# Kernel tuning notes

Measured on AMD Instinct MI355X. Metric: run time of the kernel, lower is better.

## Reference

```python
import jax, jax.numpy as jnp
import numpy as np

EPS = 1e-5

def _layernorm(x, gamma, beta):
    mu = jnp.mean(x, axis=-1, keepdims=True)
    var = jnp.var(x, axis=-1, keepdims=True)
    return (x - mu) * jax.lax.rsqrt(var + EPS) * gamma + beta

def setup_inputs() -> dict:
    key = jax.random.key(0)
    ks = jax.random.split(key, 8)
    B, N, c_z, c_h = 1, 384, 128, 128
    s_z = 1.0 / np.sqrt(c_z)
    s_h = 1.0 / np.sqrt(c_h)
    return {
        "z_ij": jax.random.normal(ks[0], (B, N, N, c_z), dtype=jnp.float32),
        "ln_in_g": jnp.ones((c_z,), jnp.float32),
        "ln_in_b": jnp.zeros((c_z,), jnp.float32),
        "ln_out_g": jnp.ones((c_h,), jnp.float32),
        "ln_out_b": jnp.zeros((c_h,), jnp.float32),
        "Wa1": jax.random.uniform(ks[1], (c_h, c_z), jnp.float32, -s_z, s_z),
        "Wa2": jax.random.uniform(ks[2], (c_h, c_z), jnp.float32, -s_z, s_z),
        "Wb1": jax.random.uniform(ks[3], (c_h, c_z), jnp.float32, -s_z, s_z),
        "Wb2": jax.random.uniform(ks[4], (c_h, c_z), jnp.float32, -s_z, s_z),
        "Wg": jax.random.uniform(ks[5], (c_z, c_z), jnp.float32, -s_z, s_z),
        "Wout": jax.random.uniform(ks[6], (c_z, c_h), jnp.float32, -s_h, s_h),
    }

def reference(z_ij, ln_in_g, ln_in_b, ln_out_g, ln_out_b, Wa1, Wa2, Wb1, Wb2, Wg, Wout):
    # Algorithm 12: triangular multiplicative update, "outgoing" edges
    z = _layernorm(z_ij, ln_in_g, ln_in_b)              # [B,N,N,c_z]
    a = jax.nn.sigmoid(z @ Wa1.T) * (z @ Wa2.T)         # [B,N,N,c_h]
    b = jax.nn.sigmoid(z @ Wb1.T) * (z @ Wb2.T)         # [B,N,N,c_h]
    g = jax.nn.sigmoid(z @ Wg.T)                        # [B,N,N,c_z]
    s = jnp.einsum('bikd,bjkd->bijd', a, b)             # pairwise contraction over k
    return g * (_layernorm(s, ln_out_g, ln_out_b) @ Wout.T)
```

## Files before the change

kernel.cpp:

```cpp
#include <hip/hip_runtime.h>
#include <stdint.h>

#define N 384
#define NR (N*N)
#define PL (NR + 64)
#define C 128
#define WSZ 16384

typedef unsigned short ushort_t;
typedef __attribute__((ext_vector_type(8))) _Float16 f16x8;
typedef __attribute__((ext_vector_type(4))) float f32x4;

__device__ __forceinline__ ushort_t f2h(float f) {
  union { _Float16 h; ushort_t u; } v; v.h = (_Float16)f; return v.u;
}
__device__ __forceinline__ void unpack8h(uint4 q, float f[8]) {
  union { uint4 q; _Float16 h[8]; } v; v.q = q;
#pragma unroll
  for (int e = 0; e < 8; ++e) f[e] = (float)v.h[e];
}
__device__ __forceinline__ uint4 pack8h(const float f[8]) {
  union { uint4 q; _Float16 h[8]; } v;
#pragma unroll
  for (int e = 0; e < 8; ++e) v.h[e] = (_Float16)f[e];
  return v.q;
}

__device__ __forceinline__ float bf2f(ushort_t u) {
  union { unsigned int i; float f; } v; v.i = ((unsigned int)u) << 16; return v.f;
}
__device__ __forceinline__ ushort_t f2bf(float f) {
  union { float f; unsigned int i; } v; v.f = f;
  unsigned int u = v.i + 0x7FFF + ((v.i >> 16) & 1);
  return (ushort_t)(u >> 16);
}
__device__ __forceinline__ void unpack8bf(uint4 q, float f[8]) {
  const unsigned int* w = (const unsigned int*)&q;
#pragma unroll
  for (int e = 0; e < 4; ++e) {
    f[2*e]   = bf2f((ushort_t)(w[e] & 0xffffu));
    f[2*e+1] = bf2f((ushort_t)(w[e] >> 16));
  }
}
__device__ __forceinline__ uint4 pack8bf(const float f[8]) {
  uint4 q;
  unsigned int* w = (unsigned int*)&q;
#pragma unroll
  for (int e = 0; e < 4; ++e)
    w[e] = (unsigned int)f2bf(f[2*e]) | ((unsigned int)f2bf(f[2*e+1]) << 16);
  return q;
}

__device__ __forceinline__ float sigmoidf_(float x) {
  return __builtin_amdgcn_rcpf(1.0f + __expf(-x));
}

__device__ __forceinline__ void load8f(const void* p, size_t idx, int isf32, float f[8]) {
  if (isf32) {
    const float* q = (const float*)p + idx;
    const float4 a = ((const float4*)q)[0];
    const float4 b = ((const float4*)q)[1];
    f[0]=a.x; f[1]=a.y; f[2]=a.z; f[3]=a.w;
    f[4]=b.x; f[5]=b.y; f[6]=b.z; f[7]=b.w;
  } else {
    unpack8bf(*(const uint4*)((const ushort_t*)p + idx), f);
  }
}
__device__ __forceinline__ void store8(void* p, size_t idx, int isf32, const float f[8]) {
  if (isf32) {
    float* q = (float*)p + idx;
    ((float4*)q)[0] = make_float4(f[0], f[1], f[2], f[3]);
    ((float4*)q)[1] = make_float4(f[4], f[5], f[6], f[7]);
  } else {
    *(uint4*)((ushort_t*)p + idx) = pack8bf(f);
  }
}
__device__ __forceinline__ void store1(void* p, size_t idx, int isf32, float v) {
  if (isf32) ((float*)p)[idx] = v;
  else       ((ushort_t*)p)[idx] = f2bf(v);
}

__global__ __launch_bounds__(256, 4)
void k0(const unsigned int* __restrict__ zw, const void* __restrict__ z,
        const void* __restrict__ gin, const void* __restrict__ bin,
        const void* __restrict__ Wa1, const void* __restrict__ Wa2,
        const void* __restrict__ Wb1, const void* __restrict__ Wb2,
        const void* __restrict__ Wg,  const void* __restrict__ Wout,
        ushort_t* __restrict__ wp, ushort_t* __restrict__ zn,
        int* __restrict__ flag)
{
  const int t = threadIdx.x;
  __shared__ int cnt[4];
  {
    unsigned int u = zw[t];
    int e = (u >> 23) & 0xFF;
    int sane = (e >= 87 && e <= 132) ? 1 : 0;
    unsigned long long b = __ballot(sane);
    if ((t & 63) == 0) cnt[t >> 6] = __popcll(b);
  }
  __syncthreads();
  const int isf32 = ((cnt[0] + cnt[1] + cnt[2] + cnt[3]) >= 128) ? 1 : 0;
  const int bid = blockIdx.x;
  if (bid == 0 && t == 0) flag[0] = isf32;

  if (bid < 6) {
    const void* src;
    switch (bid) {
      case 0: src = Wa1; break;
      case 1: src = Wa2; break;
      case 2: src = Wb1; break;
      case 3: src = Wb2; break;
      case 4: src = Wg;  break;
      default: src = Wout; break;
    }
    ushort_t* dst = wp + (size_t)bid * WSZ;
    for (int c = t; c < 2048; c += 256) {
      int ks = c >> 9, nf = (c >> 6) & 7, lane = c & 63;
      int quad = lane >> 4, l16 = lane & 15;
      size_t sidx = (size_t)(nf*16 + l16)*128 + ks*32 + quad*8;
      float f[8]; load8f(src, sidx, isf32, f);
      *(uint4*)(dst + (size_t)c*8) = pack8h(f);
    }
    return;
  }

  const int tid = (bid - 6) * 256 + t;
  const int r = tid >> 2, h = tid & 3;
  float x[4][8];
  float sum = 0.f, sq = 0.f;
#pragma unroll
  for (int j = 0; j < 4; ++j) {
    load8f(z, (size_t)r*C + h*32 + j*8, isf32, x[j]);
#pragma unroll
    for (int e = 0; e < 8; ++e) { sum += x[j][e]; sq += x[j][e]*x[j][e]; }
  }
  sum += __shfl_xor(sum, 1); sum += __shfl_xor(sum, 2);
  sq  += __shfl_xor(sq, 1);  sq  += __shfl_xor(sq, 2);
  const float mu = sum * 0.0078125f;
  const float rstd = rsqrtf(sq * 0.0078125f - mu*mu + 1e-5f);
#pragma unroll
  for (int j = 0; j < 4; ++j) {
    float ga[8], be[8];
    load8f(gin, (size_t)(h*32 + j*8), isf32, ga);
    load8f(bin, (size_t)(h*32 + j*8), isf32, be);
    float f[8];
#pragma unroll
    for (int e = 0; e < 8; ++e) f[e] = (x[j][e] - mu) * rstd * ga[e] + be[e];
    *(uint4*)(zn + (size_t)r*C + h*32 + j*8) = pack8h(f);
  }
}

__global__ __launch_bounds__(256, 2)
void k1b(const ushort_t* __restrict__ zn, const ushort_t* __restrict__ wp,
         ushort_t* __restrict__ a_t, ushort_t* __restrict__ b_t,
         void* __restrict__ gout, ushort_t* __restrict__ g_t, int gIsWs,
         const int* __restrict__ flag)
{
  __shared__ ushort_t tb[128*72];
  const int t = threadIdx.x;
  const int isf32 = *flag;
  const int wave = t >> 6, lane = t & 63;
  const int quad = lane >> 4, l16 = lane & 15;
  const int rg = wave >> 1, ch = wave & 1;
  const int R0 = blockIdx.x * 64;
  const f32x4 z4 = {0.f, 0.f, 0.f, 0.f};

  f16x8 af[2][4];
#pragma unroll
  for (int mf = 0; mf < 2; ++mf) {
    const int row = R0 + rg*32 + mf*16 + l16;
#pragma unroll
    for (int ks = 0; ks < 4; ++ks)
      af[mf][ks] = *(const f16x8*)(zn + (size_t)row*C + ks*32 + quad*8);
  }

  auto pair = [&](const ushort_t* W1p, const ushort_t* W2p, ushort_t* dst) {
#pragma unroll 1
    for (int nh = 0; nh < 2; ++nh) {
      f32x4 a1[2][2], a2[2][2];
#pragma unroll
      for (int mf = 0; mf < 2; ++mf)
#pragma unroll
        for (int nn = 0; nn < 2; ++nn) { a1[mf][nn] = z4; a2[mf][nn] = z4; }
#pragma unroll
      for (int ks = 0; ks < 4; ++ks)
#pragma unroll
        for (int nn = 0; nn < 2; ++nn) {
          const size_t foff = (size_t)((ks*8 + ch*4 + nh*2 + nn)*64 + lane) * 8;
          f16x8 b1 = *(const f16x8*)(W1p + foff);
          f16x8 b2 = *(const f16x8*)(W2p + foff);
#pragma unroll
          for (int mf = 0; mf < 2; ++mf) {
            a1[mf][nn] = __builtin_amdgcn_mfma_f32_16x16x32_f16(af[mf][ks], b1, a1[mf][nn], 0, 0, 0);
            a2[mf][nn] = __builtin_amdgcn_mfma_f32_16x16x32_f16(af[mf][ks], b2, a2[mf][nn], 0, 0, 0);
          }
        }
#pragma unroll
      for (int mf = 0; mf < 2; ++mf)
#pragma unroll
        for (int nn = 0; nn < 2; ++nn)
#pragma unroll
          for (int r = 0; r < 4; ++r) {
            int rowl = rg*32 + mf*16 + quad*4 + r;
            int col  = ch*64 + (nh*2 + nn)*16 + l16;
            tb[col*72 + rowl] = f2h(a2[mf][nn][r] * sigmoidf_(a1[mf][nn][r]));
          }
    }
    asm volatile("s_waitcnt lgkmcnt(0)" ::: "memory");
    __builtin_amdgcn_s_barrier();
#pragma unroll
    for (int i = 0; i < 4; ++i) {
      int cid = t + i*256, dl = cid >> 3, rc = cid & 7;
      uint4 v = *(const uint4*)(tb + dl*72 + rc*8);
      *(uint4*)(dst + (size_t)dl*PL + R0 + rc*8) = v;
    }
    asm volatile("" ::: "memory");
    __builtin_amdgcn_s_barrier();
  };
  pair(wp + 0*WSZ, wp + 1*WSZ, a_t);
  pair(wp + 2*WSZ, wp + 3*WSZ, b_t);

  {
    const ushort_t* Wgp = wp + 4*WSZ;
    f32x4 ag[2][4];
#pragma unroll
    for (int mf = 0; mf < 2; ++mf)
#pragma unroll
      for (int nf = 0; nf < 4; ++nf) ag[mf][nf] = z4;
#pragma unroll
    for (int ks = 0; ks < 4; ++ks)
#pragma unroll
      for (int nf = 0; nf < 4; ++nf) {
        const size_t foff = (size_t)((ks*8 + ch*4 + nf)*64 + lane) * 8;
        f16x8 b = *(const f16x8*)(Wgp + foff);
#pragma unroll
        for (int mf = 0; mf < 2; ++mf)
          ag[mf][nf] = __builtin_amdgcn_mfma_f32_16x16x32_f16(af[mf][ks], b, ag[mf][nf], 0, 0, 0);
      }
#pragma unroll
    for (int mf = 0; mf < 2; ++mf)
#pragma unroll
      for (int nf = 0; nf < 4; ++nf)
#pragma unroll
        for (int r = 0; r < 4; ++r) {
          int row = R0 + rg*32 + mf*16 + quad*4 + r;
          int col = ch*64 + nf*16 + l16;
          float v = sigmoidf_(ag[mf][nf][r]);
          size_t idx = (size_t)row*C + col;
          if (gIsWs) g_t[idx] = f2h(v);
          else       store1(gout, idx, isf32, v);
        }
  }
}

__global__ __launch_bounds__(256, 3)
void k2(const ushort_t* __restrict__ a_t, const ushort_t* __restrict__ b_t,
        ushort_t* __restrict__ s_t)
{
  __shared__ ushort_t As[128*64];
  __shared__ ushort_t Bs[128*64];
  const int t = threadIdx.x;
  const int wave = t >> 6, lane = t & 63;
  const int quad = lane >> 4, l16 = lane & 15;
  const int wm = wave >> 1, wn = wave & 1;
  const int lin = blockIdx.x;
  const int xcd = lin & 7, slot = lin >> 3;
  const int d = xcd + 8*(slot/9);
  const int tile = slot - (slot/9)*9;
  const int i0 = (tile/3) * 128, j0 = (tile%3) * 128;
  const size_t dbase = (size_t)d * PL;

  f32x4 acc[4][4];
  const f32x4 z4 = {0.f, 0.f, 0.f, 0.f};
#pragma unroll
  for (int mf = 0; mf < 4; ++mf)
#pragma unroll
    for (int nf = 0; nf < 4; ++nf) acc[mf][nf] = z4;

  uint4 va[4], vb[4];
#pragma unroll
  for (int j = 0; j < 4; ++j) {
    int cid = t + j*256, row = cid >> 3, c = cid & 7;
    va[j] = *(const uint4*)(a_t + dbase + (size_t)(i0 + row)*N + c*8);
    vb[j] = *(const uint4*)(b_t + dbase + (size_t)(j0 + row)*N + c*8);
  }

  for (int kt = 0; kt < 6; ++kt) {
#pragma unroll
    for (int j = 0; j < 4; ++j) {
      int cid = t + j*256, row = cid >> 3, c = cid & 7;
      int p = c ^ (row & 7);
      *(uint4*)(As + row*64 + p*8) = va[j];
      *(uint4*)(Bs + row*64 + p*8) = vb[j];
    }
    if (kt < 5) {
#pragma unroll
      for (int j = 0; j < 4; ++j) {
        int cid = t + j*256, row = cid >> 3, c = cid & 7;
        va[j] = *(const uint4*)(a_t + dbase + (size_t)(i0 + row)*N + (kt+1)*64 + c*8);
        vb[j] = *(const uint4*)(b_t + dbase + (size_t)(j0 + row)*N + (kt+1)*64 + c*8);
      }
    }
    asm volatile("s_waitcnt lgkmcnt(0)" ::: "memory");
    __builtin_amdgcn_s_barrier();

#pragma unroll
    for (int ks = 0; ks < 2; ++ks) {
      f16x8 afr[4], bfr[4];
#pragma unroll
      for (int f = 0; f < 4; ++f) {
        int ra = wm*64 + f*16 + l16;
        int pa = (ks*4 + quad) ^ (ra & 7);
        afr[f] = *(const f16x8*)(As + ra*64 + pa*8);
        int rb = wn*64 + f*16 + l16;
        int pb = (ks*4 + quad) ^ (rb & 7);
        bfr[f] = *(const f16x8*)(Bs + rb*64 + pb*8);
      }
#pragma unroll
      for (int mf = 0; mf < 4; ++mf)
#pragma unroll
        for (int nf = 0; nf < 4; ++nf)
          acc[mf][nf] = __builtin_amdgcn_mfma_f32_16x16x32_f16(afr[mf], bfr[nf], acc[mf][nf], 0, 0, 0);
    }
    asm volatile("" ::: "memory");
    __builtin_amdgcn_s_barrier();
  }
#pragma unroll
  for (int mf = 0; mf < 4; ++mf)
#pragma unroll
    for (int nf = 0; nf < 4; ++nf)
#pragma unroll
      for (int r = 0; r < 4; ++r) {
        int row = wm*64 + mf*16 + quad*4 + r;
        int col = wn*64 + nf*16 + l16;
        s_t[dbase + (size_t)(i0 + row)*N + j0 + col] = f2h(acc[mf][nf][r]);
      }
}

__global__ __launch_bounds__(256, 2)
void k3(const ushort_t* __restrict__ s_t, const void* __restrict__ gno,
        const void* __restrict__ bno, const ushort_t* __restrict__ wp,
        void* __restrict__ io, const ushort_t* __restrict__ g_t, int gIsWs,
        const int* __restrict__ flag)
{
  __shared__ ushort_t ss[64*136];
  __shared__ float muA[64];
  __shared__ float rsA[64];
  const int t = threadIdx.x;
  const int isf32 = *flag;
  const int wave = t >> 6, lane = t & 63;
  const int quad = lane >> 4, l16 = lane & 15;
  const int R0 = blockIdx.x * 64;
  const ushort_t* Woutp = wp + 5*WSZ;

  {
    const int dg = t >> 3, rg = t & 7;
    const int d0 = dg * 4;
    uint4 v[4];
#pragma unroll
    for (int dd = 0; dd < 4; ++dd)
      v[dd] = *(const uint4*)(s_t + (size_t)(d0 + dd)*PL + R0 + rg*8);
    const ushort_t* sv = (const ushort_t*)v;
#pragma unroll
    for (int rr0 = 0; rr0 < 8; ++rr0) {
      int rr = (rr0 + (t & 7)) & 7;
      alignas(8) ushort_t w[4];
#pragma unroll
      for (int dd = 0; dd < 4; ++dd) w[dd] = sv[dd*8 + rr];
      *(uint2*)(ss + (rg*8 + rr)*136 + d0) = *(const uint2*)w;
    }
  }
  asm volatile("s_waitcnt lgkmcnt(0)" ::: "memory");
  __builtin_amdgcn_s_barrier();

  {
    const int r = t >> 2, h = t & 3;
    float sum = 0.f, sq = 0.f;
#pragma unroll
    for (int j = 0; j < 4; ++j) {
      uint4 q = *(const uint4*)(ss + r*136 + h*32 + j*8);
      float f[8]; unpack8h(q, f);
#pragma unroll
      for (int e = 0; e < 8; ++e) { sum += f[e]; sq += f[e]*f[e]; }
    }
    sum += __shfl_xor(sum, 1); sum += __shfl_xor(sum, 2);
    sq  += __shfl_xor(sq, 1);  sq  += __shfl_xor(sq, 2);
    if (h == 0) {
      const float mu = sum * 0.0078125f;
      muA[r] = mu;
      rsA[r] = rsqrtf(sq * 0.0078125f - mu*mu + 1e-5f);
    }
  }
  asm volatile("s_waitcnt lgkmcnt(0)" ::: "memory");
  __builtin_amdgcn_s_barrier();

  f16x8 afr[4];
  {
    const int frow = wave*16 + l16;
    const float mu_r = muA[frow];
    const float rs_r = rsA[frow];
#pragma unroll
    for (int ks = 0; ks < 4; ++ks) {
      uint4 raw = *(const uint4*)(ss + frow*136 + (ks*4 + quad)*8);
      float f[8], ga[8], be[8];
      unpack8h(raw, f);
      load8f(gno, (size_t)(ks*32 + quad*8), isf32, ga);
      load8f(bno, (size_t)(ks*32 + quad*8), isf32, be);
      union { alignas(16) _Float16 h[8]; f16x8 v; } u;
#pragma unroll
      for (int e = 0; e < 8; ++e)
        u.h[e] = (_Float16)((f[e] - mu_r) * rs_r * ga[e] + be[e]);
      afr[ks] = u.v;
    }
  }
  asm volatile("s_waitcnt lgkmcnt(0)" ::: "memory");
  __builtin_amdgcn_s_barrier();

  const f32x4 z4 = {0.f, 0.f, 0.f, 0.f};
#pragma unroll 1
  for (int nh = 0; nh < 2; ++nh) {
    f32x4 acc[4];
#pragma unroll
    for (int nn = 0; nn < 4; ++nn) acc[nn] = z4;
#pragma unroll
    for (int ks = 0; ks < 4; ++ks)
#pragma unroll
      for (int nn = 0; nn < 4; ++nn) {
        size_t foff = (size_t)(((ks*8 + nh*4 + nn)*64 + lane)) * 8;
        f16x8 b = *(const f16x8*)(Woutp + foff);
        acc[nn] = __builtin_amdgcn_mfma_f32_16x16x32_f16(afr[ks], b, acc[nn], 0, 0, 0);
      }
#pragma unroll
    for (int nn = 0; nn < 4; ++nn)
#pragma unroll
      for (int r = 0; r < 4; ++r) {
        int row = wave*16 + quad*4 + r;
        int col = (nh*4 + nn)*16 + l16;
        ss[row*136 + col] = f2h(acc[nn][r]);
      }
  }
  asm volatile("s_waitcnt lgkmcnt(0)" ::: "memory");
  __builtin_amdgcn_s_barrier();

#pragma unroll
  for (int i = 0; i < 4; ++i) {
    int cid = t + i*256;
    int row = cid >> 4, ch = cid & 15;
    size_t idx = (size_t)(R0 + row)*C + ch*8;
    float gf[8], hf[8], of[8];
    if (gIsWs) unpack8h(*(const uint4*)(g_t + idx), gf);
    else       load8f(io, idx, isf32, gf);
    unpack8h(*(const uint4*)(ss + row*136 + ch*8), hf);
#pragma unroll
    for (int e = 0; e < 8; ++e) of[e] = gf[e] * hf[e];
    store8(io, idx, isf32, of);
  }
}

extern "C" void kernel_launch(void* const* d_in, const int* in_sizes, int n_in,
                              void* d_out, int out_size, void* d_ws, size_t ws_size,
                              hipStream_t stream) {
  (void)in_sizes; (void)n_in; (void)out_size;
  const void* z    = d_in[0];
  const void* gin  = d_in[1];
  const void* bin  = d_in[2];
  const void* gno  = d_in[3];
  const void* bno  = d_in[4];
  const void* Wa1  = d_in[5];
  const void* Wa2  = d_in[6];
  const void* Wb1  = d_in[7];
  const void* Wb2  = d_in[8];
  const void* Wg   = d_in[9];
  const void* Wout = d_in[10];

  const size_t plane = (size_t)C * PL;
  int* flag     = (int*)d_ws;
  ushort_t* wp  = (ushort_t*)((char*)d_ws + 256);
  ushort_t* a_t = wp + (size_t)6*WSZ;
  ushort_t* b_t = a_t + plane;
  ushort_t* s_t = b_t + plane;
  ushort_t* g_t = s_t + plane;
  size_t need_g = 256 + (size_t)6*WSZ*2 + (3*plane + (size_t)NR*C)*2;
  int gIsWs = (ws_size >= need_g) ? 1 : 0;

  ushort_t* zn = s_t;

  k0<<<6 + NR*4/256, 256, 0, stream>>>((const unsigned int*)z, z, gin, bin,
                                       Wa1, Wa2, Wb1, Wb2, Wg, Wout, wp, zn, flag);
  k1b<<<NR/64, 256, 0, stream>>>(zn, wp, a_t, b_t, d_out, g_t, gIsWs, flag);
  k2<<<1152, 256, 0, stream>>>(a_t, b_t, s_t);
  k3<<<NR/64, 256, 0, stream>>>(s_t, gno, bno, wp, d_out, g_t, gIsWs, flag);
}
```

Measured before the change: 297.5 us.

## Fuse input layernorm into projection kernel and stage gate stores through LDS

The input layernorm now runs inside the projection kernel instead of a separate kernel that wrote normalized fp16 z to global memory and read it back. Each block loads its 64 rows of z into LDS, computes per-row mean and rstd there, and applies gamma/beta while building the MFMA A fragments. The former prep kernel only repacks the weights and sets the dtype flag. Gate outputs are staged through LDS so the global stores are coalesced 16-byte writes instead of scattered scalar ones. The cost is more LDS per block and statistics computed from fp16-rounded inputs, which slightly changes precision.

```diff
diff --git a/kernel.cpp b/kernel.cpp
--- a/kernel.cpp
+++ b/kernel.cpp
@@ -75,19 +75,12 @@
     *(uint4*)((ushort_t*)p + idx) = pack8bf(f);
   }
 }
-__device__ __forceinline__ void store1(void* p, size_t idx, int isf32, float v) {
-  if (isf32) ((float*)p)[idx] = v;
-  else       ((ushort_t*)p)[idx] = f2bf(v);
-}
-
-__global__ __launch_bounds__(256, 4)
-void k0(const unsigned int* __restrict__ zw, const void* __restrict__ z,
-        const void* __restrict__ gin, const void* __restrict__ bin,
-        const void* __restrict__ Wa1, const void* __restrict__ Wa2,
-        const void* __restrict__ Wb1, const void* __restrict__ Wb2,
-        const void* __restrict__ Wg,  const void* __restrict__ Wout,
-        ushort_t* __restrict__ wp, ushort_t* __restrict__ zn,
-        int* __restrict__ flag)
+
+__global__ void kprep(const unsigned int* __restrict__ zw,
+                      const void* __restrict__ Wa1, const void* __restrict__ Wa2,
+                      const void* __restrict__ Wb1, const void* __restrict__ Wb2,
+                      const void* __restrict__ Wg,  const void* __restrict__ Wout,
+                      ushort_t* __restrict__ wp, int* __restrict__ flag)
 {
   const int t = threadIdx.x;
   __shared__ int cnt[4];
@@ -100,63 +93,38 @@
   }
   __syncthreads();
   const int isf32 = ((cnt[0] + cnt[1] + cnt[2] + cnt[3]) >= 128) ? 1 : 0;
-  const int bid = blockIdx.x;
-  if (bid == 0 && t == 0) flag[0] = isf32;
-
-  if (bid < 6) {
-    const void* src;
-    switch (bid) {
-      case 0: src = Wa1; break;
-      case 1: src = Wa2; break;
-      case 2: src = Wb1; break;
-      case 3: src = Wb2; break;
-      case 4: src = Wg;  break;
-      default: src = Wout; break;
-    }
-    ushort_t* dst = wp + (size_t)bid * WSZ;
-    for (int c = t; c < 2048; c += 256) {
-      int ks = c >> 9, nf = (c >> 6) & 7, lane = c & 63;
-      int quad = lane >> 4, l16 = lane & 15;
-      size_t sidx = (size_t)(nf*16 + l16)*128 + ks*32 + quad*8;
-      float f[8]; load8f(src, sidx, isf32, f);
-      *(uint4*)(dst + (size_t)c*8) = pack8h(f);
-    }
-    return;
-  }
-
-  const int tid = (bid - 6) * 256 + t;
-  const int r = tid >> 2, h = tid & 3;
-  float x[4][8];
-  float sum = 0.f, sq = 0.f;
-#pragma unroll
-  for (int j = 0; j < 4; ++j) {
-    load8f(z, (size_t)r*C + h*32 + j*8, isf32, x[j]);
-#pragma unroll
-    for (int e = 0; e < 8; ++e) { sum += x[j][e]; sq += x[j][e]*x[j][e]; }
-  }
-  sum += __shfl_xor(sum, 1); sum += __shfl_xor(sum, 2);
-  sq  += __shfl_xor(sq, 1);  sq  += __shfl_xor(sq, 2);
-  const float mu = sum * 0.0078125f;
-  const float rstd = rsqrtf(sq * 0.0078125f - mu*mu + 1e-5f);
-#pragma unroll
-  for (int j = 0; j < 4; ++j) {
-    float ga[8], be[8];
-    load8f(gin, (size_t)(h*32 + j*8), isf32, ga);
-    load8f(bin, (size_t)(h*32 + j*8), isf32, be);
-    float f[8];
-#pragma unroll
-    for (int e = 0; e < 8; ++e) f[e] = (x[j][e] - mu) * rstd * ga[e] + be[e];
-    *(uint4*)(zn + (size_t)r*C + h*32 + j*8) = pack8h(f);
+  if (blockIdx.x == 0 && t == 0) flag[0] = isf32;
+
+  const void* src;
+  switch (blockIdx.x) {
+    case 0: src = Wa1; break;
+    case 1: src = Wa2; break;
+    case 2: src = Wb1; break;
+    case 3: src = Wb2; break;
+    case 4: src = Wg;  break;
+    default: src = Wout; break;
+  }
+  ushort_t* dst = wp + (size_t)blockIdx.x * WSZ;
+  for (int c = t; c < 2048; c += 256) {
+    int ks = c >> 9, nf = (c >> 6) & 7, lane = c & 63;
+    int quad = lane >> 4, l16 = lane & 15;
+    size_t sidx = (size_t)(nf*16 + l16)*128 + ks*32 + quad*8;
+    float f[8]; load8f(src, sidx, isf32, f);
+    *(uint4*)(dst + (size_t)c*8) = pack8h(f);
   }
 }
 
 __global__ __launch_bounds__(256, 2)
-void k1b(const ushort_t* __restrict__ zn, const ushort_t* __restrict__ wp,
+void k1b(const void* __restrict__ z, const void* __restrict__ gin,
+         const void* __restrict__ bin, const ushort_t* __restrict__ wp,
          ushort_t* __restrict__ a_t, ushort_t* __restrict__ b_t,
          void* __restrict__ gout, ushort_t* __restrict__ g_t, int gIsWs,
          const int* __restrict__ flag)
 {
+  __shared__ ushort_t zz[64*136];
   __shared__ ushort_t tb[128*72];
+  __shared__ float muA[64];
+  __shared__ float rsA[64];
   const int t = threadIdx.x;
   const int isf32 = *flag;
   const int wave = t >> 6, lane = t & 63;
@@ -165,13 +133,56 @@
   const int R0 = blockIdx.x * 64;
   const f32x4 z4 = {0.f, 0.f, 0.f, 0.f};
 
+#pragma unroll
+  for (int i = 0; i < 4; ++i) {
+    int cid = t + i*256, row = cid >> 4, chk = cid & 15;
+    float f[8];
+    load8f(z, (size_t)(R0 + row)*C + chk*8, isf32, f);
+    *(uint4*)(zz + row*136 + chk*8) = pack8h(f);
+  }
+  asm volatile("s_waitcnt lgkmcnt(0)" ::: "memory");
+  __builtin_amdgcn_s_barrier();
+
+  {
+    const int r = t >> 2, h = t & 3;
+    float sum = 0.f, sq = 0.f;
+#pragma unroll
+    for (int j = 0; j < 4; ++j) {
+      uint4 q = *(const uint4*)(zz + r*136 + h*32 + j*8);
+      float f[8]; unpack8h(q, f);
+#pragma unroll
+      for (int e = 0; e < 8; ++e) { sum += f[e]; sq += f[e]*f[e]; }
+    }
+    sum += __shfl_xor(sum, 1); sum += __shfl_xor(sum, 2);
+    sq  += __shfl_xor(sq, 1);  sq  += __shfl_xor(sq, 2);
+    if (h == 0) {
+      const float mu = sum * 0.0078125f;
+      muA[r] = mu;
+      rsA[r] = rsqrtf(sq * 0.0078125f - mu*mu + 1e-5f);
+    }
+  }
+  asm volatile("s_waitcnt lgkmcnt(0)" ::: "memory");
+  __builtin_amdgcn_s_barrier();
+
   f16x8 af[2][4];
 #pragma unroll
   for (int mf = 0; mf < 2; ++mf) {
-    const int row = R0 + rg*32 + mf*16 + l16;
-#pragma unroll
-    for (int ks = 0; ks < 4; ++ks)
-      af[mf][ks] = *(const f16x8*)(zn + (size_t)row*C + ks*32 + quad*8);
+    const int rowl = rg*32 + mf*16 + l16;
+    const float mu_r = muA[rowl];
+    const float rs_r = rsA[rowl];
+#pragma unroll
+    for (int ks = 0; ks < 4; ++ks) {
+      uint4 raw = *(const uint4*)(zz + rowl*136 + ks*32 + quad*8);
+      float x[8], ga[8], be[8];
+      unpack8h(raw, x);
+      load8f(gin, (size_t)(ks*32 + quad*8), isf32, ga);
+      load8f(bin, (size_t)(ks*32 + quad*8), isf32, be);
+      union { alignas(16) _Float16 h[8]; f16x8 v; } u;
+#pragma unroll
+      for (int e = 0; e < 8; ++e)
+        u.h[e] = (_Float16)((x[e] - mu_r) * rs_r * ga[e] + be[e]);
+      af[mf][ks] = u.v;
+    }
   }
 
   auto pair = [&](const ushort_t* W1p, const ushort_t* W2p, ushort_t* dst) {
@@ -243,13 +254,24 @@
       for (int nf = 0; nf < 4; ++nf)
 #pragma unroll
         for (int r = 0; r < 4; ++r) {
-          int row = R0 + rg*32 + mf*16 + quad*4 + r;
-          int col = ch*64 + nf*16 + l16;
-          float v = sigmoidf_(ag[mf][nf][r]);
-          size_t idx = (size_t)row*C + col;
-          if (gIsWs) g_t[idx] = f2h(v);
-          else       store1(gout, idx, isf32, v);
+          int rowl = rg*32 + mf*16 + quad*4 + r;
+          int col  = ch*64 + nf*16 + l16;
+          tb[rowl*136 + col] = f2h(sigmoidf_(ag[mf][nf][r]));
         }
+    asm volatile("s_waitcnt lgkmcnt(0)" ::: "memory");
+    __builtin_amdgcn_s_barrier();
+#pragma unroll
+    for (int i = 0; i < 4; ++i) {
+      int cid = t + i*256, row = cid >> 4, chk = cid & 15;
+      uint4 v = *(const uint4*)(tb + row*136 + chk*8);
+      size_t idx = (size_t)(R0 + row)*C + chk*8;
+      if (gIsWs) {
+        *(uint4*)(g_t + idx) = v;
+      } else {
+        float f[8]; unpack8h(v, f);
+        store8(gout, idx, isf32, f);
+      }
+    }
   }
 }
 
@@ -483,11 +505,8 @@
   size_t need_g = 256 + (size_t)6*WSZ*2 + (3*plane + (size_t)NR*C)*2;
   int gIsWs = (ws_size >= need_g) ? 1 : 0;
 
-  ushort_t* zn = s_t;
-
-  k0<<<6 + NR*4/256, 256, 0, stream>>>((const unsigned int*)z, z, gin, bin,
-                                       Wa1, Wa2, Wb1, Wb2, Wg, Wout, wp, zn, flag);
-  k1b<<<NR/64, 256, 0, stream>>>(zn, wp, a_t, b_t, d_out, g_t, gIsWs, flag);
+  kprep<<<6, 256, 0, stream>>>((const unsigned int*)z, Wa1, Wa2, Wb1, Wb2, Wg, Wout, wp, flag);
+  k1b<<<NR/64, 256, 0, stream>>>(z, gin, bin, wp, a_t, b_t, d_out, g_t, gIsWs, flag);
   k2<<<1152, 256, 0, stream>>>(a_t, b_t, s_t);
   k3<<<NR/64, 256, 0, stream>>>(s_t, gno, bno, wp, d_out, g_t, gIsWs, flag);
 }
```

Result: no change. 293.5 us (-1.4%).
